# Kernel optimization log

Hardware: AMD Instinct MI355X
Metric: run time of the kernel (lower is better)

The kernel has to match this reference:

```python
import jax, jax.numpy as jnp
import numpy as np

N_ITEM = 100000
DIV_TRADEOFF = 0.1


def setup_inputs() -> dict:
    key = jax.random.key(0)
    ks = jax.random.split(key, 9)
    B, K, L, D_LLM, H = 512, 8, 50, 768, 128
    return {
        "user_id": jax.random.randint(ks[0], (B,), 0, 50000),
        "base_model_preds": jax.random.randint(ks[1], (B, K, L), 0, N_ITEM + 1),
        "preference_in": jax.random.normal(ks[2], (B, H), jnp.float32),
        "pos_label": jax.random.normal(ks[3], (B, K), jnp.float32),
        "neg_label": jax.random.normal(ks[4], (B, K), jnp.float32),
        "user_embeddings": jax.random.normal(ks[5], (50000, H), jnp.float32) * 0.01,
        "item_embeddings": jax.random.normal(ks[6], (N_ITEM + 1, D_LLM), jnp.float32) * 0.02,
        "W_proj": jax.random.normal(ks[7], (D_LLM, H), jnp.float32) * (1.0 / np.sqrt(D_LLM)),
        "b_proj": jax.random.normal(ks[8], (H,), jnp.float32) * 0.01,
    }


def reference(user_id, base_model_preds, preference_in, pos_label, neg_label,
              user_embeddings, item_embeddings, W_proj, b_proj):
    B, K, L = base_model_preds.shape
    # masked gather-embed: ids outside (0, n_item] map to a zero row
    valid = (base_model_preds > 0) & (base_model_preds <= N_ITEM)
    safe_ids = jnp.where(valid, base_model_preds, 0)
    focus_llm = item_embeddings[safe_ids] * valid[..., None].astype(item_embeddings.dtype)  # [B,K,L,D_llm]
    # linear projection to hidden (bias applied everywhere, matching nn.Linear on zeroed rows)
    bm = jnp.einsum('bkld,dh->bklh', focus_llm, W_proj) + b_proj  # [B,K,L,H]
    # time-decay weighted sum over sequence positions
    time_w = 1.0 / jnp.log2(jnp.arange(L, dtype=jnp.float32) + 2.0)  # [L]
    basemodel_emb = jnp.einsum('bklh,l->bkh', bm, time_w)  # [B,K,H]
    # preference = DIEN(...) + user_emb  (DIEN output modeled by preference_in)
    preference = preference_in + user_embeddings[user_id]  # [B,H]
    wgts_org = jnp.einsum('bkh,bh->bk', basemodel_emb, preference)
    wgts = jax.nn.softmax(wgts_org, axis=-1)  # [B,K]
    pos_scores = jnp.sum(pos_label * wgts, axis=1)
    neg_scores = jnp.sum(neg_label * wgts, axis=1)
    loss = -jnp.sum(jax.nn.log_sigmoid(pos_scores - neg_scores))
    # diversity regularizer (use_div=True)
    cov_wgt = jax.lax.stop_gradient(wgts[:, None, :] + wgts[:, :, None])  # [B,K,K]
    cov_mask = 1.0 - jnp.eye(K, dtype=wgts.dtype)  # [K,K]
    gram = jnp.einsum('bih,bjh->bij', basemodel_emb, basemodel_emb) ** 2
    loss_div = DIV_TRADEOFF * jnp.mean(cov_mask[None] * gram * cov_wgt)
    return loss + loss_div
```

## Files before the change

kernel.cpp:

```cpp
#include <hip/hip_runtime.h>
#include <math.h>

#define B_SZ 512
#define K_SZ 8
#define L_SZ 50
#define DLLM 768
#define H_SZ 128
#define N_ITEM 100000
#define DIV_TRADEOFF 0.1f
#define M_PAD 100032

typedef float  f32x4 __attribute__((ext_vector_type(4)));
typedef short  bf16x8 __attribute__((ext_vector_type(8)));
typedef unsigned int u32x4 __attribute__((ext_vector_type(4)));
typedef unsigned short u16x8 __attribute__((ext_vector_type(8)));

__device__ __forceinline__ unsigned short f2bf(float f) {
    unsigned u = __float_as_uint(f);
    u += 0x7fffu + ((u >> 16) & 1u);
    return (unsigned short)(u >> 16);
}

__device__ __forceinline__ void gload_lds16(const void* g, void* l) {
    __builtin_amdgcn_global_load_lds(
        (const __attribute__((address_space(1))) unsigned*)g,
        (__attribute__((address_space(3))) unsigned*)l, 16, 0, 0);
}

__global__ __launch_bounds__(256) void k_wt(
    const float* __restrict__ W,
    unsigned short* __restrict__ Wt,
    float* __restrict__ out)
{
    __shared__ float tile[64][65];
    const int kb = blockIdx.x >> 1;
    const int nb = blockIdx.x & 1;
    const int t  = threadIdx.x;
    if (blockIdx.x == 0 && t == 0) out[0] = 0.0f;

    const int r  = t >> 2;
    const int c0 = (t & 3) * 16;
    #pragma unroll
    for (int j = 0; j < 4; ++j) {
        const float4 v = *(const float4*)(W + (size_t)(kb * 64 + r) * H_SZ + nb * 64 + c0 + j * 4);
        tile[r][c0 + j * 4 + 0] = v.x;
        tile[r][c0 + j * 4 + 1] = v.y;
        tile[r][c0 + j * 4 + 2] = v.z;
        tile[r][c0 + j * 4 + 3] = v.w;
    }
    __syncthreads();
    const int n  = t >> 2;
    const int k0 = (t & 3) * 16;
    u16x8 lo, hi;
    #pragma unroll
    for (int j = 0; j < 8; ++j) lo[j] = f2bf(tile[k0 + j][n]);
    #pragma unroll
    for (int j = 0; j < 8; ++j) hi[j] = f2bf(tile[k0 + 8 + j][n]);
    unsigned short* dst = Wt + (size_t)(nb * 64 + n) * DLLM + kb * 64 + k0;
    *(u16x8*)(dst)     = lo;
    *(u16x8*)(dst + 8) = hi;
}

__global__ __launch_bounds__(256) void k_proj(
    const float* __restrict__ item,
    const unsigned short* __restrict__ Wt,
    unsigned short* __restrict__ projb)
{
    __shared__ float          As[2][64 * 64];
    __shared__ unsigned short Bs[2][128 * 64];

    const int t    = threadIdx.x;
    const int brow = blockIdx.x * 64;
    const int w    = t >> 6;
    const int lane = t & 63;
    const int nl   = lane & 15;
    const int g    = lane >> 4;
    const int key  = nl & 7;

    const int a_rsub = (lane >> 4);
    const int a_gl   = lane & 15;
    const int b_nsub = (lane >> 3);
    const int b_gl   = lane & 7;
    const int b_key  = b_nsub & 7;

    const int r = w * 16 + nl;

    auto STAGE = [&](int d, int c) {
        const int kc = c * 64;
        #pragma unroll
        for (int i = 0; i < 4; ++i) {
            const int row_t = w * 16 + i * 4 + a_rsub;
            const int rowS  = (brow + row_t <= N_ITEM) ? (brow + row_t) : N_ITEM;
            const int ka    = (a_gl ^ (row_t & 7)) * 4;
            gload_lds16(item + (size_t)rowS * DLLM + kc + ka,
                        &As[d][w * 1024 + i * 256]);
        }
        #pragma unroll
        for (int i = 0; i < 4; ++i) {
            const int n_t = w * 32 + i * 8 + b_nsub;
            const int kb  = (b_gl ^ b_key) * 8;
            gload_lds16(Wt + (size_t)n_t * DLLM + kc + kb,
                        &Bs[d][w * 2048 + i * 512]);
        }
    };

    f32x4 acc[8];
    #pragma unroll
    for (int i = 0; i < 8; ++i) acc[i] = (f32x4){0.f, 0.f, 0.f, 0.f};

    STAGE(0, 0);

    for (int c = 0; c < 12; ++c) {
        const int cur = c & 1;
        if (c < 11) STAGE(cur ^ 1, c + 1);
        if (c < 11) asm volatile("s_waitcnt vmcnt(8)" ::: "memory");
        else        asm volatile("s_waitcnt vmcnt(0)" ::: "memory");
        __builtin_amdgcn_s_barrier();
        __builtin_amdgcn_sched_barrier(0);

        #pragma unroll
        for (int ks = 0; ks < 2; ++ks) {
            const f32x4 alo = *(const f32x4*)&As[cur][r * 64 + 4 * ((ks * 8 + 2 * g)     ^ key)];
            const f32x4 ahi = *(const f32x4*)&As[cur][r * 64 + 4 * ((ks * 8 + 2 * g + 1) ^ key)];
            unsigned p0, p1, p2, p3;
            asm("v_cvt_pk_bf16_f32 %0, %1, %2" : "=v"(p0) : "v"(alo.x), "v"(alo.y));
            asm("v_cvt_pk_bf16_f32 %0, %1, %2" : "=v"(p1) : "v"(alo.z), "v"(alo.w));
            asm("v_cvt_pk_bf16_f32 %0, %1, %2" : "=v"(p2) : "v"(ahi.x), "v"(ahi.y));
            asm("v_cvt_pk_bf16_f32 %0, %1, %2" : "=v"(p3) : "v"(ahi.z), "v"(ahi.w));
            union { u32x4 u; bf16x8 s; } af;
            af.u[0] = p0; af.u[1] = p1; af.u[2] = p2; af.u[3] = p3;

            #pragma unroll
            for (int nt = 0; nt < 8; ++nt) {
                const bf16x8 b = *(const bf16x8*)&Bs[cur][(nt * 16 + nl) * 64
                                                          + 8 * ((ks * 4 + g) ^ key)];
                acc[nt] = __builtin_amdgcn_mfma_f32_16x16x32_bf16(af.s, b, acc[nt], 0, 0, 0);
            }
        }
        asm volatile("s_waitcnt lgkmcnt(0)" ::: "memory");
        __builtin_amdgcn_s_barrier();
        __builtin_amdgcn_sched_barrier(0);
    }

    const int rbase = brow + w * 16 + 4 * g;
    #pragma unroll
    for (int nt = 0; nt < 8; ++nt) {
        #pragma unroll
        for (int rr = 0; rr < 4; ++rr) {
            projb[(size_t)(rbase + rr) * H_SZ + nt * 16 + nl] = f2bf(acc[nt][rr]);
        }
    }
}

__global__ __launch_bounds__(512) void k_gloss(
    const int* __restrict__ preds,
    const unsigned short* __restrict__ projb,
    const float* __restrict__ bproj,
    const int* __restrict__ user_id, const float* __restrict__ pref_in,
    const float* __restrict__ pos_label, const float* __restrict__ neg_label,
    const float* __restrict__ user_emb,
    float* __restrict__ out)
{
    const int b    = blockIdx.x;
    const int tid  = threadIdx.x;
    const int wv   = tid >> 6;
    const int lane = tid & 63;
    const int h2   = lane * 2;

    __shared__ float e[K_SZ][H_SZ + 1];
    __shared__ float pref[H_SZ];
    __shared__ float sdot[K_SZ];
    __shared__ float wg[K_SZ];
    __shared__ float lossb_s;

    {
        const int* __restrict__ p = preds + ((size_t)b * K_SZ + wv) * L_SZ;
        constexpr int PF = 8;
        unsigned buf[PF];
        float wgt[PF];
        #pragma unroll
        for (int i = 0; i < PF; ++i) {
            const int id = p[i];
            const bool v = (id > 0) && (id <= N_ITEM);
            wgt[i] = v ? (1.0f / log2f((float)(i + 2))) : 0.0f;
            buf[i] = *(const unsigned*)(projb + (size_t)(v ? id : 0) * H_SZ + h2);
        }
        float a0 = 0.f, a1 = 0.f;
        #pragma unroll
        for (int l = 0; l < L_SZ; ++l) {
            const int s = l % PF;
            const unsigned u = buf[s];
            const float w = wgt[s];
            if (l + PF < L_SZ) {
                const int id = p[l + PF];
                const bool v = (id > 0) && (id <= N_ITEM);
                wgt[s] = v ? (1.0f / log2f((float)(l + PF + 2))) : 0.0f;
                buf[s] = *(const unsigned*)(projb + (size_t)(v ? id : 0) * H_SZ + h2);
            }
            a0 += w * __uint_as_float(u << 16);
            a1 += w * __uint_as_float(u & 0xffff0000u);
        }
        float sumw = 0.f;
        #pragma unroll
        for (int l = 0; l < L_SZ; ++l) sumw += 1.0f / log2f((float)(l + 2));
        e[wv][h2]     = a0 + bproj[h2]     * sumw;
        e[wv][h2 + 1] = a1 + bproj[h2 + 1] * sumw;
    }
    if (tid < H_SZ) {
        const int uid = user_id[b];
        pref[tid] = pref_in[(size_t)b * H_SZ + tid] + user_emb[(size_t)uid * H_SZ + tid];
    }
    __syncthreads();

    if (tid < 256) {
        const int k = tid >> 5;
        const int l32 = tid & 31;
        float s = e[k][l32] * pref[l32] + e[k][l32 + 32] * pref[l32 + 32]
                + e[k][l32 + 64] * pref[l32 + 64] + e[k][l32 + 96] * pref[l32 + 96];
        #pragma unroll
        for (int m = 16; m >= 1; m >>= 1) s += __shfl_xor(s, m, 64);
        if (l32 == 0) sdot[k] = s;
    }
    __syncthreads();

    if (tid == 0) {
        float mx = sdot[0];
        #pragma unroll
        for (int k = 1; k < K_SZ; ++k) mx = fmaxf(mx, sdot[k]);
        float sum = 0.f; float ex[K_SZ];
        #pragma unroll
        for (int k = 0; k < K_SZ; ++k) { ex[k] = expf(sdot[k] - mx); sum += ex[k]; }
        float ps = 0.f, ns = 0.f;
        #pragma unroll
        for (int k = 0; k < K_SZ; ++k) {
            const float w = ex[k] / sum;
            wg[k] = w;
            ps += pos_label[(size_t)b * K_SZ + k] * w;
            ns += neg_label[(size_t)b * K_SZ + k] * w;
        }
        const float x = ps - ns;
        lossb_s = fmaxf(-x, 0.f) + log1pf(expf(-fabsf(x)));
    }
    __syncthreads();

    if (tid < 64) {
        const int i = tid >> 3;
        const int j = tid & 7;
        float gsum = 0.f;
        for (int h = 0; h < H_SZ; ++h) gsum += e[i][h] * e[j][h];
        float v = (i != j) ? (gsum * gsum * (wg[i] + wg[j])) : 0.f;
        #pragma unroll
        for (int m = 32; m >= 1; m >>= 1) v += __shfl_xor(v, m, 64);
        if (tid == 0) {
            const float mean_div = v / (float)(B_SZ * K_SZ * K_SZ);
            atomicAdd(out, lossb_s + DIV_TRADEOFF * mean_div);
        }
    }
}

__global__ __launch_bounds__(192) void k_gather_fb(
    const int* __restrict__ preds, const float* __restrict__ item,
    float* __restrict__ wf, float* __restrict__ out)
{
    const int bk  = blockIdx.x;
    const int tid = threadIdx.x;
    if (bk == 0 && tid == 0) out[0] = 0.0f;
    const int* __restrict__ p = preds + (size_t)bk * L_SZ;
    const float* __restrict__ ibase = item + (size_t)tid * 4;
    float4 acc = make_float4(0.f, 0.f, 0.f, 0.f);
    constexpr int PF = 8;
    float4 buf[PF]; float wgt[PF];
    #pragma unroll
    for (int i = 0; i < PF; ++i) {
        const int id = p[i];
        const bool v = (id > 0) && (id <= N_ITEM);
        wgt[i] = v ? (1.0f / log2f((float)(i + 2))) : 0.0f;
        buf[i] = *(const float4*)(ibase + (size_t)(v ? id : 0) * DLLM);
    }
    #pragma unroll
    for (int l = 0; l < L_SZ; ++l) {
        const int s = l % PF;
        const float4 v4 = buf[s];
        const float  w  = wgt[s];
        if (l + PF < L_SZ) {
            const int id = p[l + PF];
            const bool v = (id > 0) && (id <= N_ITEM);
            wgt[s] = v ? (1.0f / log2f((float)(l + PF + 2))) : 0.0f;
            buf[s] = *(const float4*)(ibase + (size_t)(v ? id : 0) * DLLM);
        }
        acc.x += w * v4.x; acc.y += w * v4.y; acc.z += w * v4.z; acc.w += w * v4.w;
    }
    *(float4*)(wf + (size_t)bk * DLLM + (size_t)tid * 4) = acc;
}

__global__ __launch_bounds__(256) void k_projloss_fb(
    const float* __restrict__ wf, const float* __restrict__ W,
    const float* __restrict__ bproj, const int* __restrict__ user_id,
    const float* __restrict__ pref_in, const float* __restrict__ pos_label,
    const float* __restrict__ neg_label, const float* __restrict__ user_emb,
    float* __restrict__ out)
{
    const int b   = blockIdx.x;
    const int tid = threadIdx.x;
    const int c   = tid & (H_SZ - 1);
    const int rg  = tid >> 7;
    __shared__ float A[K_SZ][H_SZ];
    __shared__ float e[K_SZ][H_SZ + 1];
    __shared__ float pref[H_SZ];
    __shared__ float sdot[K_SZ];
    __shared__ float wg[K_SZ];
    __shared__ float lossb_s;
    float acc[4] = {0.f, 0.f, 0.f, 0.f};
    const size_t rowbase = (size_t)b * K_SZ;
    for (int kb = 0; kb < DLLM; kb += H_SZ) {
        __syncthreads();
        {
            const int r  = tid >> 5;
            const int kk = (tid & 31) * 4;
            *(float4*)&A[r][kk] = *(const float4*)(wf + (rowbase + r) * DLLM + kb + kk);
        }
        __syncthreads();
        #pragma unroll 4
        for (int k = 0; k < H_SZ; k += 4) {
            const float4 a0 = *(const float4*)&A[rg][k];
            const float4 a1 = *(const float4*)&A[rg + 2][k];
            const float4 a2 = *(const float4*)&A[rg + 4][k];
            const float4 a3 = *(const float4*)&A[rg + 6][k];
            const float* Wp = W + (size_t)(kb + k) * H_SZ + c;
            const float w0 = Wp[0]; const float w1 = Wp[H_SZ];
            const float w2 = Wp[2 * H_SZ]; const float w3 = Wp[3 * H_SZ];
            acc[0] += a0.x * w0 + a0.y * w1 + a0.z * w2 + a0.w * w3;
            acc[1] += a1.x * w0 + a1.y * w1 + a1.z * w2 + a1.w * w3;
            acc[2] += a2.x * w0 + a2.y * w1 + a2.z * w2 + a2.w * w3;
            acc[3] += a3.x * w0 + a3.y * w1 + a3.z * w2 + a3.w * w3;
        }
    }
    float sumw = 0.f;
    #pragma unroll
    for (int l = 0; l < L_SZ; ++l) sumw += 1.0f / log2f((float)(l + 2));
    const float bterm = bproj[c] * sumw;
    #pragma unroll
    for (int ri = 0; ri < 4; ++ri) e[rg + 2 * ri][c] = acc[ri] + bterm;
    if (tid < H_SZ) {
        const int uid = user_id[b];
        pref[tid] = pref_in[(size_t)b * H_SZ + tid] + user_emb[(size_t)uid * H_SZ + tid];
    }
    __syncthreads();
    {
        const int k    = tid >> 5;
        const int lane = tid & 31;
        float s = e[k][lane] * pref[lane] + e[k][lane + 32] * pref[lane + 32]
                + e[k][lane + 64] * pref[lane + 64] + e[k][lane + 96] * pref[lane + 96];
        #pragma unroll
        for (int m = 16; m >= 1; m >>= 1) s += __shfl_xor(s, m, 64);
        if (lane == 0) sdot[k] = s;
    }
    __syncthreads();
    if (tid == 0) {
        float mx = sdot[0];
        #pragma unroll
        for (int k = 1; k < K_SZ; ++k) mx = fmaxf(mx, sdot[k]);
        float sum = 0.f; float ex[K_SZ];
        #pragma unroll
        for (int k = 0; k < K_SZ; ++k) { ex[k] = expf(sdot[k] - mx); sum += ex[k]; }
        float ps = 0.f, ns = 0.f;
        #pragma unroll
        for (int k = 0; k < K_SZ; ++k) {
            const float w = ex[k] / sum;
            wg[k] = w;
            ps += pos_label[(size_t)b * K_SZ + k] * w;
            ns += neg_label[(size_t)b * K_SZ + k] * w;
        }
        const float x = ps - ns;
        lossb_s = fmaxf(-x, 0.f) + log1pf(expf(-fabsf(x)));
    }
    __syncthreads();
    if (tid < 64) {
        const int i = tid >> 3;
        const int j = tid & 7;
        float g = 0.f;
        for (int h = 0; h < H_SZ; ++h) g += e[i][h] * e[j][h];
        float v = (i != j) ? (g * g * (wg[i] + wg[j])) : 0.f;
        #pragma unroll
        for (int m = 32; m >= 1; m >>= 1) v += __shfl_xor(v, m, 64);
        if (tid == 0) {
            const float mean_div = v / (float)(B_SZ * K_SZ * K_SZ);
            atomicAdd(out, lossb_s + DIV_TRADEOFF * mean_div);
        }
    }
}

extern "C" void kernel_launch(void* const* d_in, const int* in_sizes, int n_in,
                              void* d_out, int out_size, void* d_ws, size_t ws_size,
                              hipStream_t stream) {
    const int*   user_id   = (const int*)  d_in[0];
    const int*   preds     = (const int*)  d_in[1];
    const float* pref_in   = (const float*)d_in[2];
    const float* pos_label = (const float*)d_in[3];
    const float* neg_label = (const float*)d_in[4];
    const float* user_emb  = (const float*)d_in[5];
    const float* item_emb  = (const float*)d_in[6];
    const float* W_proj    = (const float*)d_in[7];
    const float* b_proj    = (const float*)d_in[8];

    float* out = (float*)d_out;

    const size_t projb_bytes = (size_t)M_PAD * H_SZ * sizeof(unsigned short);
    const size_t wt_off      = projb_bytes;
    const size_t wt_bytes    = (size_t)H_SZ * DLLM * sizeof(unsigned short);
    const size_t need        = wt_off + wt_bytes;

    if (ws_size >= need) {
        unsigned short* projb = (unsigned short*)d_ws;
        unsigned short* Wt    = (unsigned short*)((char*)d_ws + wt_off);

        k_wt<<<24, 256, 0, stream>>>(W_proj, Wt, out);
        k_proj<<<M_PAD / 64, 256, 0, stream>>>(item_emb, Wt, projb);
        k_gloss<<<B_SZ, 512, 0, stream>>>(preds, projb, b_proj, user_id, pref_in,
                                          pos_label, neg_label, user_emb, out);
    } else {
        float* wf = (float*)d_ws;
        k_gather_fb<<<B_SZ * K_SZ, 192, 0, stream>>>(preds, item_emb, wf, out);
        k_projloss_fb<<<B_SZ, 256, 0, stream>>>(wf, W_proj, b_proj, user_id, pref_in,
                                                pos_label, neg_label, user_emb, out);
    }
}
```

Before: 104.4 us.

## Triple-buffer item tiles and prefetch A two chunks ahead in projection GEMM

Splits the staging lambda into separate A (item rows) and B (weights) loads, triple-buffers the fp32 item tile in LDS, and issues A loads two k-chunks ahead while B stays double-buffered one chunk ahead. The aim is to hide more of the global-memory latency of the large item-embedding stream behind MFMA work. The cost is extra LDS (another 16KB As buffer), which can lower occupancy, plus more complex vmcnt bookkeeping with an extra barrier per iteration.

```diff
diff --git a/kernel.cpp b/kernel.cpp
--- a/kernel.cpp
+++ b/kernel.cpp
@@ -66,7 +66,7 @@
     const unsigned short* __restrict__ Wt,
     unsigned short* __restrict__ projb)
 {
-    __shared__ float          As[2][64 * 64];
+    __shared__ float          As[3][64 * 64];
     __shared__ unsigned short Bs[2][128 * 64];
 
     const int t    = threadIdx.x;
@@ -85,7 +85,7 @@
 
     const int r = w * 16 + nl;
 
-    auto STAGE = [&](int d, int c) {
+    auto STAGE_A = [&](int d, int c) {
         const int kc = c * 64;
         #pragma unroll
         for (int i = 0; i < 4; ++i) {
@@ -95,6 +95,9 @@
             gload_lds16(item + (size_t)rowS * DLLM + kc + ka,
                         &As[d][w * 1024 + i * 256]);
         }
+    };
+    auto STAGE_B = [&](int d, int c) {
+        const int kc = c * 64;
         #pragma unroll
         for (int i = 0; i < 4; ++i) {
             const int n_t = w * 32 + i * 8 + b_nsub;
@@ -108,20 +111,24 @@
     #pragma unroll
     for (int i = 0; i < 8; ++i) acc[i] = (f32x4){0.f, 0.f, 0.f, 0.f};
 
-    STAGE(0, 0);
+    STAGE_A(0, 0);
+    STAGE_B(0, 0);
+    STAGE_A(1, 1);
+    asm volatile("s_waitcnt vmcnt(4)" ::: "memory");
+    __builtin_amdgcn_s_barrier();
+    __builtin_amdgcn_sched_barrier(0);
 
     for (int c = 0; c < 12; ++c) {
-        const int cur = c & 1;
-        if (c < 11) STAGE(cur ^ 1, c + 1);
-        if (c < 11) asm volatile("s_waitcnt vmcnt(8)" ::: "memory");
-        else        asm volatile("s_waitcnt vmcnt(0)" ::: "memory");
-        __builtin_amdgcn_s_barrier();
+        if (c + 1 < 12) STAGE_B((c + 1) & 1, c + 1);
+        if (c + 2 < 12) STAGE_A((c + 2) % 3, c + 2);
         __builtin_amdgcn_sched_barrier(0);
 
+        const float*          Asc = &As[c % 3][0];
+        const unsigned short* Bsc = &Bs[c & 1][0];
         #pragma unroll
         for (int ks = 0; ks < 2; ++ks) {
-            const f32x4 alo = *(const f32x4*)&As[cur][r * 64 + 4 * ((ks * 8 + 2 * g)     ^ key)];
-            const f32x4 ahi = *(const f32x4*)&As[cur][r * 64 + 4 * ((ks * 8 + 2 * g + 1) ^ key)];
+            const f32x4 alo = *(const f32x4*)&Asc[r * 64 + 4 * ((ks * 8 + 2 * g)     ^ key)];
+            const f32x4 ahi = *(const f32x4*)&Asc[r * 64 + 4 * ((ks * 8 + 2 * g + 1) ^ key)];
             unsigned p0, p1, p2, p3;
             asm("v_cvt_pk_bf16_f32 %0, %1, %2" : "=v"(p0) : "v"(alo.x), "v"(alo.y));
             asm("v_cvt_pk_bf16_f32 %0, %1, %2" : "=v"(p1) : "v"(alo.z), "v"(alo.w));
@@ -132,14 +139,25 @@
 
             #pragma unroll
             for (int nt = 0; nt < 8; ++nt) {
-                const bf16x8 b = *(const bf16x8*)&Bs[cur][(nt * 16 + nl) * 64
-                                                          + 8 * ((ks * 4 + g) ^ key)];
+                const bf16x8 b = *(const bf16x8*)&Bsc[(nt * 16 + nl) * 64
+                                                      + 8 * ((ks * 4 + g) ^ key)];
                 acc[nt] = __builtin_amdgcn_mfma_f32_16x16x32_bf16(af.s, b, acc[nt], 0, 0, 0);
             }
         }
+
         asm volatile("s_waitcnt lgkmcnt(0)" ::: "memory");
         __builtin_amdgcn_s_barrier();
         __builtin_amdgcn_sched_barrier(0);
+
+        if (c < 10) {
+            asm volatile("s_waitcnt vmcnt(4)" ::: "memory");
+            __builtin_amdgcn_s_barrier();
+            __builtin_amdgcn_sched_barrier(0);
+        } else if (c == 10) {
+            asm volatile("s_waitcnt vmcnt(0)" ::: "memory");
+            __builtin_amdgcn_s_barrier();
+            __builtin_amdgcn_sched_barrier(0);
+        }
     }
 
     const int rbase = brow + w * 16 + 4 * g;
```

Measured after the change: 104.4 us. No clear change (+0.0%).
